# Performance work log

Measured on AMD Instinct MI355X. Metric: run time of the kernel, lower is better.

Reference implementation:

```python
import jax, jax.numpy as jnp
import numpy as np

N = 50000
NEG_SLOPE = 0.2
EPS = 1e-16


def add_self_loops(edge_index, n):
    loop = jnp.arange(n, dtype=edge_index.dtype)
    src = jnp.concatenate([edge_index[0], loop])
    dst = jnp.concatenate([edge_index[1], loop])
    return src, dst


def gat_conv(x, src, dst, W, att_src, att_dst, bias, n):
    # x: [N, F_in]; W: [F_in, H*D]; att_*: [H, D]; bias: [H*D]
    H, D = att_src.shape
    h = (x @ W).reshape(n, H, D)                      # [N, H, D]
    a_src = jnp.einsum('nhd,hd->nh', h, att_src)      # [N, H]
    a_dst = jnp.einsum('nhd,hd->nh', h, att_dst)
    e = jax.nn.leaky_relu(a_src[src] + a_dst[dst], NEG_SLOPE)  # [E, H]
    # softmax over incoming edges per destination node, per head
    m = jax.ops.segment_max(e, dst, num_segments=n)   # [N, H]
    ex = jnp.exp(e - m[dst])
    s = jax.ops.segment_sum(ex, dst, num_segments=n)
    alpha = ex / (s[dst] + EPS)                       # [E, H]
    msg = h[src] * alpha[:, :, None]                  # [E, H, D]
    out = jax.ops.segment_sum(msg, dst, num_segments=n)
    return out.reshape(n, H * D) + bias


def gcn_conv(x, src, dst, W, bias, n):
    h = x @ W                                         # [N, C]
    deg = jax.ops.segment_sum(jnp.ones_like(src, dtype=h.dtype), dst, num_segments=n)
    dinv = jnp.where(deg > 0, jax.lax.rsqrt(deg), 0.0)
    norm = dinv[src] * dinv[dst]                      # [E]
    out = jax.ops.segment_sum(h[src] * norm[:, None], dst, num_segments=n)
    return out + bias


def setup_inputs() -> dict:
    key = jax.random.key(0)
    ks = jax.random.split(key, 12)
    F_in, hid, heads, ncls = 128, 32, 8, 8
    d2 = hid // 2  # 16
    E = 500000
    x = jax.random.normal(ks[0], (N, F_in), dtype=jnp.float32)
    edge_index = jax.random.randint(ks[1], (2, E), 0, N, dtype=jnp.int32)
    sc = lambda k, sh: jax.random.normal(k, sh, dtype=jnp.float32) * 0.05
    return {
        'x': x, 'edge_index': edge_index,
        'W1': sc(ks[2], (F_in, heads * hid)),
        'att_src1': sc(ks[3], (heads, hid)), 'att_dst1': sc(ks[4], (heads, hid)),
        'b1': jnp.zeros((heads * hid,), jnp.float32),
        'W2': sc(ks[5], (heads * hid, heads * d2)),
        'att_src2': sc(ks[6], (heads, d2)), 'att_dst2': sc(ks[7], (heads, d2)),
        'b2': jnp.zeros((heads * d2,), jnp.float32),
        'Wg': sc(ks[8], (heads * d2, ncls)),
        'bg': jnp.zeros((ncls,), jnp.float32),
    }


def reference(x, edge_index, W1, att_src1, att_dst1, b1, W2, att_src2, att_dst2, b2, Wg, bg):
    src, dst = add_self_loops(edge_index, N)
    h = gat_conv(x, src, dst, W1, att_src1, att_dst1, b1, N)
    h = jax.nn.relu(h)
    h = gat_conv(h, src, dst, W2, att_src2, att_dst2, b2, N)
    h = jax.nn.relu(h)
    return gcn_conv(h, src, dst, Wg, bg, N)
```

## Files before the change

kernel.cpp:

```cpp
#include <hip/hip_runtime.h>
#include <hip/hip_bf16.h>


typedef __attribute__((ext_vector_type(8))) short bf16x8;
typedef __attribute__((ext_vector_type(4))) float f32x4;


__global__ __launch_bounds__(256) void zero_deg_kernel(int* __restrict__ deg, int n) {
    int i = blockIdx.x * 256 + threadIdx.x;
    if (i < n) deg[i] = 0;
}

__global__ __launch_bounds__(256) void hist_kernel(const int* __restrict__ ei, int E, int Etot,
                                                   int* __restrict__ deg) {
    int e = blockIdx.x * 256 + threadIdx.x;
    if (e >= Etot) return;
    int d = (e < E) ? ei[E + e] : (e - E);
    atomicAdd(&deg[d], 1);
}

__global__ __launch_bounds__(256) void scanA_kernel(const int* __restrict__ deg,
                                                    int* __restrict__ off,
                                                    int* __restrict__ bsum, int n) {
    __shared__ int buf[256];
    int t = threadIdx.x;
    int i = blockIdx.x * 256 + t;
    int v = (i < n) ? deg[i] : 0;
    buf[t] = v;
    __syncthreads();
    #pragma unroll
    for (int st = 1; st < 256; st <<= 1) {
        int x = (t >= st) ? buf[t - st] : 0;
        __syncthreads();
        buf[t] += x;
        __syncthreads();
    }
    if (i < n) off[i + 1] = buf[t];
    if (t == 255) bsum[blockIdx.x] = buf[255];
}

__global__ __launch_bounds__(256) void scanB_kernel(int* __restrict__ bsum, int nb) {
    __shared__ int buf[256];
    int t = threadIdx.x;
    int v = (t < nb) ? bsum[t] : 0;
    buf[t] = v;
    __syncthreads();
    #pragma unroll
    for (int st = 1; st < 256; st <<= 1) {
        int x = (t >= st) ? buf[t - st] : 0;
        __syncthreads();
        buf[t] += x;
        __syncthreads();
    }
    if (t < nb) bsum[t] = buf[t] - v;
}

__global__ __launch_bounds__(256) void scanC_kernel(const int* __restrict__ deg,
                                                    int* __restrict__ off,
                                                    const int* __restrict__ bsum,
                                                    int* __restrict__ cur,
                                                    float* __restrict__ dinv, int n) {
    int i = blockIdx.x * 256 + threadIdx.x;
    if (i < n) {
        int o = off[i + 1] + bsum[blockIdx.x];
        off[i + 1] = o;
        cur[i] = o - deg[i];
        dinv[i] = rsqrtf((float)deg[i]);
    }
    if (i == 0) off[0] = 0;
}

__global__ __launch_bounds__(256) void scatter_kernel(const int* __restrict__ ei, int E, int Etot,
                                                      int* __restrict__ cur,
                                                      int* __restrict__ ssrc) {
    int e = blockIdx.x * 256 + threadIdx.x;
    if (e >= Etot) return;
    int s, d;
    if (e < E) { s = ei[e]; d = ei[E + e]; }
    else       { s = e - E; d = e - E; }
    int pos = atomicAdd(&cur[d], 1);
    ssrc[pos] = s;
}


__global__ __launch_bounds__(256) void cvt_bf16_kernel(const float* __restrict__ in,
                                                       ushort* __restrict__ outb, int count) {
    int i = (blockIdx.x * 256 + threadIdx.x) * 4;
    if (i >= count) return;
    float4 v = *reinterpret_cast<const float4*>(in + i);
    ushort4 u;
    __hip_bfloat16 b0 = __float2bfloat16(v.x); u.x = *reinterpret_cast<ushort*>(&b0);
    __hip_bfloat16 b1 = __float2bfloat16(v.y); u.y = *reinterpret_cast<ushort*>(&b1);
    __hip_bfloat16 b2 = __float2bfloat16(v.z); u.z = *reinterpret_cast<ushort*>(&b2);
    __hip_bfloat16 b3 = __float2bfloat16(v.w); u.w = *reinterpret_cast<ushort*>(&b3);
    *reinterpret_cast<ushort4*>(outb + i) = u;
}

template <int K, int NC>
__global__ __launch_bounds__(256) void wtrans_kernel(const float* __restrict__ W,
                                                     ushort* __restrict__ Wt) {
    int t = blockIdx.x * 256 + threadIdx.x;
    if (t >= K * NC) return;
    int nn = t / K, k = t % K;
    __hip_bfloat16 b = __float2bfloat16(W[(size_t)k * NC + nn]);
    Wt[t] = *reinterpret_cast<ushort*>(&b);
}


template <int K, int D>
__global__ __launch_bounds__(256) void wprep_kernel(const float* __restrict__ W,
                                                    const float* __restrict__ att_s,
                                                    const float* __restrict__ att_d,
                                                    float* __restrict__ ws,
                                                    float* __restrict__ wd) {
    int t = blockIdx.x * 256 + threadIdx.x;
    if (t >= K * 8) return;
    int k = t >> 3, h = t & 7;
    const float* wrow = W + (size_t)k * (8 * D) + h * D;
    const float* as = att_s + h * D;
    const float* ad = att_d + h * D;
    float s1 = 0.f, s2 = 0.f;
    #pragma unroll
    for (int d = 0; d < D; d += 4) {
        float4 wv = *reinterpret_cast<const float4*>(wrow + d);
        float4 av = *reinterpret_cast<const float4*>(as + d);
        float4 dv = *reinterpret_cast<const float4*>(ad + d);
        s1 += wv.x * av.x + wv.y * av.y + wv.z * av.z + wv.w * av.w;
        s2 += wv.x * dv.x + wv.y * dv.y + wv.z * dv.z + wv.w * dv.w;
    }
    ws[t] = s1;
    wd[t] = s2;
}

template <int K>
__global__ __launch_bounds__(256) void adots_kernel(const float* __restrict__ X,
                                                    const float* __restrict__ ws,
                                                    const float* __restrict__ wd,
                                                    float* __restrict__ a_s,
                                                    float* __restrict__ a_d, int n) {
    int gid = blockIdx.x * 256 + threadIdx.x;
    if (gid >= n * 8) return;
    int node = gid >> 3, h = gid & 7;
    const float* xp = X + (size_t)node * K;
    float s1 = 0.f, s2 = 0.f;
    #pragma unroll 4
    for (int k = 0; k < K; k += 4) {
        float4 xv = *reinterpret_cast<const float4*>(xp + k);
        s1 += xv.x * ws[(k + 0) * 8 + h] + xv.y * ws[(k + 1) * 8 + h] +
              xv.z * ws[(k + 2) * 8 + h] + xv.w * ws[(k + 3) * 8 + h];
        s2 += xv.x * wd[(k + 0) * 8 + h] + xv.y * wd[(k + 1) * 8 + h] +
              xv.z * wd[(k + 2) * 8 + h] + xv.w * wd[(k + 3) * 8 + h];
    }
    a_s[gid] = s1;
    a_d[gid] = s2;
}


template <int K, int NC, int BN>
__global__ __launch_bounds__(256) void mfma_gemm_kernel(const ushort* __restrict__ Ab,
                                                        const ushort* __restrict__ Bt,
                                                        ushort* __restrict__ Cb, int M) {
    constexpr int BM = 128, BK = 32;
    constexpr int FN = BN / 32;
    __shared__ ushort As[BM * BK];
    __shared__ ushort Bs[BN * BK];
    const int tid = threadIdx.x;
    const int lane = tid & 63;
    const int wid = tid >> 6;
    const int bm = blockIdx.y * BM;
    const int bn = blockIdx.x * BN;
    const int wm = (wid >> 1) * 64;
    const int wn = (wid & 1) * (BN / 2);
    const int l15 = lane & 15;
    const int l4 = lane >> 4;
    f32x4 zero4 = {0.f, 0.f, 0.f, 0.f};
    f32x4 acc[4][FN];
    #pragma unroll
    for (int i = 0; i < 4; ++i)
        #pragma unroll
        for (int j = 0; j < FN; ++j) acc[i][j] = zero4;

    for (int k0 = 0; k0 < K; k0 += BK) {
        #pragma unroll
        for (int p = 0; p < 2; ++p) {
            int ci = tid + p * 256;
            int r = ci >> 2, c = ci & 3;
            int row = bm + r;
            uint4 v = make_uint4(0, 0, 0, 0);
            if (row < M) v = *reinterpret_cast<const uint4*>(&Ab[(size_t)row * K + k0 + c * 8]);
            *reinterpret_cast<uint4*>(&As[r * BK + c * 8]) = v;
        }
        #pragma unroll
        for (int p = 0; p < BN / 64; ++p) {
            int ci = tid + p * 256;
            int r = ci >> 2, c = ci & 3;
            uint4 v = *reinterpret_cast<const uint4*>(&Bt[(size_t)(bn + r) * K + k0 + c * 8]);
            *reinterpret_cast<uint4*>(&Bs[r * BK + c * 8]) = v;
        }
        __syncthreads();
        bf16x8 af[4], bfr[FN];
        #pragma unroll
        for (int i = 0; i < 4; ++i)
            af[i] = *reinterpret_cast<const bf16x8*>(&As[(wm + 16 * i + l15) * BK + l4 * 8]);
        #pragma unroll
        for (int j = 0; j < FN; ++j)
            bfr[j] = *reinterpret_cast<const bf16x8*>(&Bs[(wn + 16 * j + l15) * BK + l4 * 8]);
        #pragma unroll
        for (int i = 0; i < 4; ++i)
            #pragma unroll
            for (int j = 0; j < FN; ++j)
                acc[i][j] = __builtin_amdgcn_mfma_f32_16x16x32_bf16(af[i], bfr[j], acc[i][j], 0, 0, 0);
        __syncthreads();
    }
    #pragma unroll
    for (int i = 0; i < 4; ++i) {
        #pragma unroll
        for (int p = 0; p < 4; ++p) {
            int row = bm + wm + 16 * i + l4 * 4 + p;
            if (row < M) {
                #pragma unroll
                for (int j = 0; j < FN; ++j) {
                    __hip_bfloat16 hb = __float2bfloat16(acc[i][j][p]);
                    Cb[(size_t)row * NC + bn + wn + 16 * j + l15] = *reinterpret_cast<ushort*>(&hb);
                }
            }
        }
    }
}


#define LRELU_EXP(e) __expf((e) > 0.f ? (e) : 0.2f * (e))

__device__ __forceinline__ float4 bf4_to_f4(uint2 v) {
    float4 r;
    r.x = __uint_as_float((v.x & 0xFFFFu) << 16);
    r.y = __uint_as_float(v.x & 0xFFFF0000u);
    r.z = __uint_as_float((v.y & 0xFFFFu) << 16);
    r.w = __uint_as_float(v.y & 0xFFFF0000u);
    return r;
}

template <int C, int DH, bool DUAL>
__global__ __launch_bounds__(256) void gat_agg_kernel(const ushort* __restrict__ hfeat,
                                                      const float* __restrict__ a_src,
                                                      const float* __restrict__ a_dst,
                                                      const int* __restrict__ off,
                                                      const int* __restrict__ ssrc,
                                                      const float* __restrict__ bias,
                                                      float* __restrict__ outp,
                                                      ushort* __restrict__ outb, int n) {
    constexpr int LPN = C / 4;
    const int node = blockIdx.x * (256 / LPN) + threadIdx.x / LPN;
    if (node >= n) return;
    const int local = threadIdx.x & (LPN - 1);
    const int c0 = local * 4;
    const int h = c0 / DH;
    const float adst = a_dst[node * 8 + h];
    const int o0 = off[node], o1 = off[node + 1];
    float ax = 0.f, ay = 0.f, az = 0.f, aw = 0.f, ssum = 0.f;
    int i = o0;
    for (; i + 4 <= o1; i += 4) {
        int s0 = ssrc[i], s1 = ssrc[i + 1], s2 = ssrc[i + 2], s3 = ssrc[i + 3];
        float e0 = a_src[s0 * 8 + h], e1 = a_src[s1 * 8 + h];
        float e2 = a_src[s2 * 8 + h], e3 = a_src[s3 * 8 + h];
        uint2 r0 = *reinterpret_cast<const uint2*>(&hfeat[(size_t)s0 * C + c0]);
        uint2 r1 = *reinterpret_cast<const uint2*>(&hfeat[(size_t)s1 * C + c0]);
        uint2 r2 = *reinterpret_cast<const uint2*>(&hfeat[(size_t)s2 * C + c0]);
        uint2 r3 = *reinterpret_cast<const uint2*>(&hfeat[(size_t)s3 * C + c0]);
        float4 h0 = bf4_to_f4(r0), h1 = bf4_to_f4(r1), h2 = bf4_to_f4(r2), h3 = bf4_to_f4(r3);
        float v0 = LRELU_EXP(e0 + adst), v1 = LRELU_EXP(e1 + adst);
        float v2 = LRELU_EXP(e2 + adst), v3 = LRELU_EXP(e3 + adst);
        ssum += (v0 + v1) + (v2 + v3);
        ax += v0 * h0.x + v1 * h1.x + v2 * h2.x + v3 * h3.x;
        ay += v0 * h0.y + v1 * h1.y + v2 * h2.y + v3 * h3.y;
        az += v0 * h0.z + v1 * h1.z + v2 * h2.z + v3 * h3.z;
        aw += v0 * h0.w + v1 * h1.w + v2 * h2.w + v3 * h3.w;
    }
    for (; i < o1; ++i) {
        int s = ssrc[i];
        float e = a_src[s * 8 + h] + adst;
        float v = LRELU_EXP(e);
        uint2 rv = *reinterpret_cast<const uint2*>(&hfeat[(size_t)s * C + c0]);
        float4 hv = bf4_to_f4(rv);
        ssum += v;
        ax += v * hv.x; ay += v * hv.y; az += v * hv.z; aw += v * hv.w;
    }
    float sinv = 1.f / (ssum + 1e-16f);
    float4 bb = *reinterpret_cast<const float4*>(bias + c0);
    float4 o;
    o.x = fmaxf(ax * sinv + bb.x, 0.f);
    o.y = fmaxf(ay * sinv + bb.y, 0.f);
    o.z = fmaxf(az * sinv + bb.z, 0.f);
    o.w = fmaxf(aw * sinv + bb.w, 0.f);
    *reinterpret_cast<float4*>(&outp[(size_t)node * C + c0]) = o;
    if constexpr (DUAL) {
        ushort4 u;
        __hip_bfloat16 b0 = __float2bfloat16(o.x); u.x = *reinterpret_cast<ushort*>(&b0);
        __hip_bfloat16 b1 = __float2bfloat16(o.y); u.y = *reinterpret_cast<ushort*>(&b1);
        __hip_bfloat16 b2 = __float2bfloat16(o.z); u.z = *reinterpret_cast<ushort*>(&b2);
        __hip_bfloat16 b3 = __float2bfloat16(o.w); u.w = *reinterpret_cast<ushort*>(&b3);
        *reinterpret_cast<ushort4*>(&outb[(size_t)node * C + c0]) = u;
    }
}


__global__ __launch_bounds__(256) void gcn_gemm_kernel(const float* __restrict__ A,
                                                       const float* __restrict__ Wg,
                                                       float* __restrict__ g, int n) {
    __shared__ float W[128 * 8];
    for (int i = threadIdx.x; i < 1024; i += 256) W[i] = Wg[i];
    __syncthreads();
    int gid = blockIdx.x * 256 + threadIdx.x;
    if (gid >= n * 8) return;
    int node = gid >> 3, c = gid & 7;
    const float* ap = A + (size_t)node * 128;
    float acc = 0.f;
    #pragma unroll
    for (int k = 0; k < 128; k += 4) {
        float4 av = *reinterpret_cast<const float4*>(ap + k);
        acc += av.x * W[(k + 0) * 8 + c] + av.y * W[(k + 1) * 8 + c] +
               av.z * W[(k + 2) * 8 + c] + av.w * W[(k + 3) * 8 + c];
    }
    g[gid] = acc;
}

__global__ __launch_bounds__(256) void gcn_agg_kernel(const float* __restrict__ g,
                                                      const float* __restrict__ dinv,
                                                      const int* __restrict__ off,
                                                      const int* __restrict__ ssrc,
                                                      const float* __restrict__ bg,
                                                      float* __restrict__ outp, int n) {
    int gid = blockIdx.x * 256 + threadIdx.x;
    if (gid >= n * 8) return;
    int node = gid >> 3, c = gid & 7;
    int o0 = off[node], o1 = off[node + 1];
    float acc = 0.f;
    for (int i = o0; i < o1; ++i) {
        int s = ssrc[i];
        acc += g[(size_t)s * 8 + c] * dinv[s];
    }
    outp[gid] = acc * dinv[node] + bg[c];
}


extern "C" void kernel_launch(void* const* d_in, const int* in_sizes, int n_in,
                              void* d_out, int out_size, void* d_ws, size_t ws_size,
                              hipStream_t stream) {
    const float* x      = (const float*)d_in[0];
    const int*   ei     = (const int*)d_in[1];
    const float* W1     = (const float*)d_in[2];
    const float* att_s1 = (const float*)d_in[3];
    const float* att_d1 = (const float*)d_in[4];
    const float* b1     = (const float*)d_in[5];
    const float* W2     = (const float*)d_in[6];
    const float* att_s2 = (const float*)d_in[7];
    const float* att_d2 = (const float*)d_in[8];
    const float* b2     = (const float*)d_in[9];
    const float* Wg     = (const float*)d_in[10];
    const float* bg     = (const float*)d_in[11];
    float* out = (float*)d_out;

    const int n    = in_sizes[0] / 128;
    const int E    = in_sizes[1] / 2;
    const int Etot = E + n;

    float*  ws     = (float*)d_ws;
    float*  out1   = ws;
    float*  reg2   = out1 + (size_t)n * 256;
    float*  reg3   = reg2 + (size_t)n * 128;
    float*  reg4   = reg3 + (size_t)n * 128;
    float*  a_s    = reg4 + (size_t)n * 64;
    float*  a_d    = a_s + (size_t)n * 8;
    float*  g      = a_d + (size_t)n * 8;
    float*  dinv   = g + (size_t)n * 8;
    float*  w1s    = dinv + n;
    float*  w1d    = w1s + 1024;
    float*  w2s    = w1d + 1024;
    float*  w2d    = w2s + 2048;
    float*  w1t_f  = w2d + 2048;
    float*  w2t_f  = w1t_f + 16384;
    int*    off    = (int*)(w2t_f + 16384);
    int*    deg    = off + (n + 1);
    int*    cur    = deg + n;
    int*    ssrc   = cur + n;
    int*    bsum   = ssrc + Etot;

    ushort* out1b = (ushort*)reg2;
    ushort* h1b   = (ushort*)reg3;
    float*  out2  = reg3;
    ushort* xb    = (ushort*)reg4;
    ushort* h2b   = (ushort*)reg4;
    ushort* W1t   = (ushort*)w1t_f;
    ushort* W2t   = (ushort*)w2t_f;

    const dim3 b256(256);
    const int nch = (n + 255) / 256;

    zero_deg_kernel<<<nch, b256, 0, stream>>>(deg, n);
    hist_kernel<<<(Etot + 255) / 256, b256, 0, stream>>>(ei, E, Etot, deg);
    scanA_kernel<<<nch, b256, 0, stream>>>(deg, off, bsum, n);
    scanB_kernel<<<1, b256, 0, stream>>>(bsum, nch);
    scanC_kernel<<<nch, b256, 0, stream>>>(deg, off, bsum, cur, dinv, n);
    scatter_kernel<<<(Etot + 255) / 256, b256, 0, stream>>>(ei, E, Etot, cur, ssrc);

    wprep_kernel<128, 32><<<4, b256, 0, stream>>>(W1, att_s1, att_d1, w1s, w1d);
    wprep_kernel<256, 16><<<8, b256, 0, stream>>>(W2, att_s2, att_d2, w2s, w2d);
    cvt_bf16_kernel<<<(n * 128 / 4 + 255) / 256, b256, 0, stream>>>(x, xb, n * 128);
    wtrans_kernel<128, 256><<<(32768 + 255) / 256, b256, 0, stream>>>(W1, W1t);
    wtrans_kernel<256, 128><<<(32768 + 255) / 256, b256, 0, stream>>>(W2, W2t);

    adots_kernel<128><<<(n * 8 + 255) / 256, b256, 0, stream>>>(x, w1s, w1d, a_s, a_d, n);
    mfma_gemm_kernel<128, 256, 128><<<dim3(2, (n + 127) / 128), b256, 0, stream>>>(xb, W1t, h1b, n);
    gat_agg_kernel<256, 32, true><<<(n + 3) / 4, b256, 0, stream>>>(h1b, a_s, a_d, off, ssrc, b1, out1, out1b, n);

    adots_kernel<256><<<(n * 8 + 255) / 256, b256, 0, stream>>>(out1, w2s, w2d, a_s, a_d, n);
    mfma_gemm_kernel<256, 128, 64><<<dim3(2, (n + 127) / 128), b256, 0, stream>>>(out1b, W2t, h2b, n);
    gat_agg_kernel<128, 16, false><<<(n + 7) / 8, b256, 0, stream>>>(h2b, a_s, a_d, off, ssrc, b2, out2, nullptr, n);

    gcn_gemm_kernel<<<(n * 8 + 255) / 256, b256, 0, stream>>>(out2, Wg, g, n);
    gcn_agg_kernel<<<(n * 8 + 255) / 256, b256, 0, stream>>>(g, dinv, off, ssrc, bg, out, n);
}
```

Baseline: 280.8 us.

## Use bf16 intermediates everywhere and cooperatively load edge indices in GAT aggregation

The GAT aggregation kernels now write only bf16 outputs. The attention-dot and GCN GEMM kernels read bf16 activations instead of the fp32 copies, which removes the fp32 out1/out2 buffers and halves their read and write traffic. The edge loop in aggregation changes too: the lanes of each head group load a chunk of source indices and attention scores together and broadcast them with shuffles, so each lane no longer loads every index and score redundantly. The cost is extra bf16 rounding in the attention logits and the GCN input, plus shuffle overhead.

```diff
diff --git a/kernel.cpp b/kernel.cpp
--- a/kernel.cpp
+++ b/kernel.cpp
@@ -82,6 +82,15 @@
     ssrc[pos] = s;
 }
 
+
+__device__ __forceinline__ float4 bf4_to_f4(uint2 v) {
+    float4 r;
+    r.x = __uint_as_float((v.x & 0xFFFFu) << 16);
+    r.y = __uint_as_float(v.x & 0xFFFF0000u);
+    r.z = __uint_as_float((v.y & 0xFFFFu) << 16);
+    r.w = __uint_as_float(v.y & 0xFFFF0000u);
+    return r;
+}
 
 __global__ __launch_bounds__(256) void cvt_bf16_kernel(const float* __restrict__ in,
                                                        ushort* __restrict__ outb, int count) {
@@ -133,7 +142,7 @@
 }
 
 template <int K>
-__global__ __launch_bounds__(256) void adots_kernel(const float* __restrict__ X,
+__global__ __launch_bounds__(256) void adots_kernel(const ushort* __restrict__ Xb,
                                                     const float* __restrict__ ws,
                                                     const float* __restrict__ wd,
                                                     float* __restrict__ a_s,
@@ -141,15 +150,21 @@
     int gid = blockIdx.x * 256 + threadIdx.x;
     if (gid >= n * 8) return;
     int node = gid >> 3, h = gid & 7;
-    const float* xp = X + (size_t)node * K;
+    const ushort* xp = Xb + (size_t)node * K;
     float s1 = 0.f, s2 = 0.f;
     #pragma unroll 4
-    for (int k = 0; k < K; k += 4) {
-        float4 xv = *reinterpret_cast<const float4*>(xp + k);
-        s1 += xv.x * ws[(k + 0) * 8 + h] + xv.y * ws[(k + 1) * 8 + h] +
-              xv.z * ws[(k + 2) * 8 + h] + xv.w * ws[(k + 3) * 8 + h];
-        s2 += xv.x * wd[(k + 0) * 8 + h] + xv.y * wd[(k + 1) * 8 + h] +
-              xv.z * wd[(k + 2) * 8 + h] + xv.w * wd[(k + 3) * 8 + h];
+    for (int k = 0; k < K; k += 8) {
+        uint4 v = *reinterpret_cast<const uint4*>(xp + k);
+        float4 x0 = bf4_to_f4(make_uint2(v.x, v.y));
+        float4 x1 = bf4_to_f4(make_uint2(v.z, v.w));
+        s1 += x0.x * ws[(k + 0) * 8 + h] + x0.y * ws[(k + 1) * 8 + h] +
+              x0.z * ws[(k + 2) * 8 + h] + x0.w * ws[(k + 3) * 8 + h] +
+              x1.x * ws[(k + 4) * 8 + h] + x1.y * ws[(k + 5) * 8 + h] +
+              x1.z * ws[(k + 6) * 8 + h] + x1.w * ws[(k + 7) * 8 + h];
+        s2 += x0.x * wd[(k + 0) * 8 + h] + x0.y * wd[(k + 1) * 8 + h] +
+              x0.z * wd[(k + 2) * 8 + h] + x0.w * wd[(k + 3) * 8 + h] +
+              x1.x * wd[(k + 4) * 8 + h] + x1.y * wd[(k + 5) * 8 + h] +
+              x1.z * wd[(k + 6) * 8 + h] + x1.w * wd[(k + 7) * 8 + h];
     }
     a_s[gid] = s1;
     a_d[gid] = s2;
@@ -231,80 +246,71 @@
 
 #define LRELU_EXP(e) __expf((e) > 0.f ? (e) : 0.2f * (e))
 
-__device__ __forceinline__ float4 bf4_to_f4(uint2 v) {
-    float4 r;
-    r.x = __uint_as_float((v.x & 0xFFFFu) << 16);
-    r.y = __uint_as_float(v.x & 0xFFFF0000u);
-    r.z = __uint_as_float((v.y & 0xFFFFu) << 16);
-    r.w = __uint_as_float(v.y & 0xFFFF0000u);
-    return r;
-}
-
-template <int C, int DH, bool DUAL>
+template <int C, int DH>
 __global__ __launch_bounds__(256) void gat_agg_kernel(const ushort* __restrict__ hfeat,
                                                       const float* __restrict__ a_src,
                                                       const float* __restrict__ a_dst,
                                                       const int* __restrict__ off,
                                                       const int* __restrict__ ssrc,
                                                       const float* __restrict__ bias,
-                                                      float* __restrict__ outp,
                                                       ushort* __restrict__ outb, int n) {
     constexpr int LPN = C / 4;
+    constexpr int GS = DH / 4;
     const int node = blockIdx.x * (256 / LPN) + threadIdx.x / LPN;
     if (node >= n) return;
     const int local = threadIdx.x & (LPN - 1);
     const int c0 = local * 4;
     const int h = c0 / DH;
+    const int subl = local & (GS - 1);
     const float adst = a_dst[node * 8 + h];
     const int o0 = off[node], o1 = off[node + 1];
     float ax = 0.f, ay = 0.f, az = 0.f, aw = 0.f, ssum = 0.f;
     int i = o0;
-    for (; i + 4 <= o1; i += 4) {
-        int s0 = ssrc[i], s1 = ssrc[i + 1], s2 = ssrc[i + 2], s3 = ssrc[i + 3];
-        float e0 = a_src[s0 * 8 + h], e1 = a_src[s1 * 8 + h];
-        float e2 = a_src[s2 * 8 + h], e3 = a_src[s3 * 8 + h];
-        uint2 r0 = *reinterpret_cast<const uint2*>(&hfeat[(size_t)s0 * C + c0]);
-        uint2 r1 = *reinterpret_cast<const uint2*>(&hfeat[(size_t)s1 * C + c0]);
-        uint2 r2 = *reinterpret_cast<const uint2*>(&hfeat[(size_t)s2 * C + c0]);
-        uint2 r3 = *reinterpret_cast<const uint2*>(&hfeat[(size_t)s3 * C + c0]);
-        float4 h0 = bf4_to_f4(r0), h1 = bf4_to_f4(r1), h2 = bf4_to_f4(r2), h3 = bf4_to_f4(r3);
-        float v0 = LRELU_EXP(e0 + adst), v1 = LRELU_EXP(e1 + adst);
-        float v2 = LRELU_EXP(e2 + adst), v3 = LRELU_EXP(e3 + adst);
-        ssum += (v0 + v1) + (v2 + v3);
-        ax += v0 * h0.x + v1 * h1.x + v2 * h2.x + v3 * h3.x;
-        ay += v0 * h0.y + v1 * h1.y + v2 * h2.y + v3 * h3.y;
-        az += v0 * h0.z + v1 * h1.z + v2 * h2.z + v3 * h3.z;
-        aw += v0 * h0.w + v1 * h1.w + v2 * h2.w + v3 * h3.w;
+    const int nfull = o0 + ((o1 - o0) / GS) * GS;
+    for (; i < nfull; i += GS) {
+        int smy = ssrc[i + subl];
+        float e = a_src[smy * 8 + h] + adst;
+        float evmy = LRELU_EXP(e);
+        int sj[GS];
+        #pragma unroll
+        for (int j = 0; j < GS; ++j) sj[j] = __shfl(smy, j, GS);
+        uint2 rv[GS];
+        #pragma unroll
+        for (int j = 0; j < GS; ++j)
+            rv[j] = *reinterpret_cast<const uint2*>(&hfeat[(size_t)sj[j] * C + c0]);
+        #pragma unroll
+        for (int j = 0; j < GS; ++j) {
+            float ev = __shfl(evmy, j, GS);
+            float4 hv = bf4_to_f4(rv[j]);
+            ssum += ev;
+            ax += ev * hv.x; ay += ev * hv.y; az += ev * hv.z; aw += ev * hv.w;
+        }
     }
     for (; i < o1; ++i) {
         int s = ssrc[i];
         float e = a_src[s * 8 + h] + adst;
         float v = LRELU_EXP(e);
-        uint2 rv = *reinterpret_cast<const uint2*>(&hfeat[(size_t)s * C + c0]);
-        float4 hv = bf4_to_f4(rv);
+        uint2 rvv = *reinterpret_cast<const uint2*>(&hfeat[(size_t)s * C + c0]);
+        float4 hv = bf4_to_f4(rvv);
         ssum += v;
         ax += v * hv.x; ay += v * hv.y; az += v * hv.z; aw += v * hv.w;
     }
     float sinv = 1.f / (ssum + 1e-16f);
     float4 bb = *reinterpret_cast<const float4*>(bias + c0);
-    float4 o;
-    o.x = fmaxf(ax * sinv + bb.x, 0.f);
-    o.y = fmaxf(ay * sinv + bb.y, 0.f);
-    o.z = fmaxf(az * sinv + bb.z, 0.f);
-    o.w = fmaxf(aw * sinv + bb.w, 0.f);
-    *reinterpret_cast<float4*>(&outp[(size_t)node * C + c0]) = o;
-    if constexpr (DUAL) {
-        ushort4 u;
-        __hip_bfloat16 b0 = __float2bfloat16(o.x); u.x = *reinterpret_cast<ushort*>(&b0);
-        __hip_bfloat16 b1 = __float2bfloat16(o.y); u.y = *reinterpret_cast<ushort*>(&b1);
-        __hip_bfloat16 b2 = __float2bfloat16(o.z); u.z = *reinterpret_cast<ushort*>(&b2);
-        __hip_bfloat16 b3 = __float2bfloat16(o.w); u.w = *reinterpret_cast<ushort*>(&b3);
-        *reinterpret_cast<ushort4*>(&outb[(size_t)node * C + c0]) = u;
-    }
-}
-
-
-__global__ __launch_bounds__(256) void gcn_gemm_kernel(const float* __restrict__ A,
+    float ox = fmaxf(ax * sinv + bb.x, 0.f);
+    float oy = fmaxf(ay * sinv + bb.y, 0.f);
+    float oz = fmaxf(az * sinv + bb.z, 0.f);
+    float ow = fmaxf(aw * sinv + bb.w, 0.f);
+    ushort4 u;
+    __hip_bfloat16 b0 = __float2bfloat16(ox); u.x = *reinterpret_cast<ushort*>(&b0);
+    __hip_bfloat16 b1 = __float2bfloat16(oy); u.y = *reinterpret_cast<ushort*>(&b1);
+    __hip_bfloat16 b2 = __float2bfloat16(oz); u.z = *reinterpret_cast<ushort*>(&b2);
+    __hip_bfloat16 b3 = __float2bfloat16(ow); u.w = *reinterpret_cast<ushort*>(&b3);
+    *reinterpret_cast<ushort4*>(&outb[(size_t)node * C + c0]) = u;
+}
+
+
+__global__ __launch_bounds__(256) void gcn_gemm_kernel(const ushort* __restrict__ Ab,
                                                        const float* __restrict__ Wg,
                                                        float* __restrict__ g, int n) {
     __shared__ float W[128 * 8];
@@ -313,13 +319,17 @@
     int gid = blockIdx.x * 256 + threadIdx.x;
     if (gid >= n * 8) return;
     int node = gid >> 3, c = gid & 7;
-    const float* ap = A + (size_t)node * 128;
+    const ushort* ap = Ab + (size_t)node * 128;
     float acc = 0.f;
     #pragma unroll
-    for (int k = 0; k < 128; k += 4) {
-        float4 av = *reinterpret_cast<const float4*>(ap + k);
-        acc += av.x * W[(k + 0) * 8 + c] + av.y * W[(k + 1) * 8 + c] +
-               av.z * W[(k + 2) * 8 + c] + av.w * W[(k + 3) * 8 + c];
+    for (int k = 0; k < 128; k += 8) {
+        uint4 v = *reinterpret_cast<const uint4*>(ap + k);
+        float4 x0 = bf4_to_f4(make_uint2(v.x, v.y));
+        float4 x1 = bf4_to_f4(make_uint2(v.z, v.w));
+        acc += x0.x * W[(k + 0) * 8 + c] + x0.y * W[(k + 1) * 8 + c] +
+               x0.z * W[(k + 2) * 8 + c] + x0.w * W[(k + 3) * 8 + c] +
+               x1.x * W[(k + 4) * 8 + c] + x1.y * W[(k + 5) * 8 + c] +
+               x1.z * W[(k + 6) * 8 + c] + x1.w * W[(k + 7) * 8 + c];
     }
     g[gid] = acc;
 }
@@ -364,32 +374,31 @@
     const int E    = in_sizes[1] / 2;
     const int Etot = E + n;
 
-    float*  ws     = (float*)d_ws;
-    float*  out1   = ws;
-    float*  reg2   = out1 + (size_t)n * 256;
-    float*  reg3   = reg2 + (size_t)n * 128;
-    float*  reg4   = reg3 + (size_t)n * 128;
-    float*  a_s    = reg4 + (size_t)n * 64;
-    float*  a_d    = a_s + (size_t)n * 8;
-    float*  g      = a_d + (size_t)n * 8;
-    float*  dinv   = g + (size_t)n * 8;
-    float*  w1s    = dinv + n;
-    float*  w1d    = w1s + 1024;
-    float*  w2s    = w1d + 1024;
-    float*  w2d    = w2s + 2048;
-    float*  w1t_f  = w2d + 2048;
-    float*  w2t_f  = w1t_f + 16384;
-    int*    off    = (int*)(w2t_f + 16384);
-    int*    deg    = off + (n + 1);
-    int*    cur    = deg + n;
-    int*    ssrc   = cur + n;
-    int*    bsum   = ssrc + Etot;
-
-    ushort* out1b = (ushort*)reg2;
-    ushort* h1b   = (ushort*)reg3;
-    float*  out2  = reg3;
-    ushort* xb    = (ushort*)reg4;
-    ushort* h2b   = (ushort*)reg4;
+    float*  wsp   = (float*)d_ws;
+    float*  regA  = wsp;
+    float*  regB  = regA + (size_t)n * 128;
+    float*  regC  = regB + (size_t)n * 128;
+    float*  a_s   = regC + (size_t)n * 64;
+    float*  a_d   = a_s + (size_t)n * 8;
+    float*  g     = a_d + (size_t)n * 8;
+    float*  dinv  = g + (size_t)n * 8;
+    float*  w1s   = dinv + n;
+    float*  w1d   = w1s + 1024;
+    float*  w2s   = w1d + 1024;
+    float*  w2d   = w2s + 2048;
+    float*  w1t_f = w2d + 2048;
+    float*  w2t_f = w1t_f + 16384;
+    int*    off   = (int*)(w2t_f + 16384);
+    int*    deg   = off + (n + 1);
+    int*    cur   = deg + n;
+    int*    ssrc  = cur + n;
+    int*    bsum  = ssrc + Etot;
+
+    ushort* h1b   = (ushort*)regA;
+    ushort* out2b = (ushort*)regA;
+    ushort* out1b = (ushort*)regB;
+    ushort* xb    = (ushort*)regC;
+    ushort* h2b   = (ushort*)regC;
     ushort* W1t   = (ushort*)w1t_f;
     ushort* W2t   = (ushort*)w2t_f;
 
@@ -409,14 +418,14 @@
     wtrans_kernel<128, 256><<<(32768 + 255) / 256, b256, 0, stream>>>(W1, W1t);
     wtrans_kernel<256, 128><<<(32768 + 255) / 256, b256, 0, stream>>>(W2, W2t);
 
-    adots_kernel<128><<<(n * 8 + 255) / 256, b256, 0, stream>>>(x, w1s, w1d, a_s, a_d, n);
+    adots_kernel<128><<<(n * 8 + 255) / 256, b256, 0, stream>>>(xb, w1s, w1d, a_s, a_d, n);
     mfma_gemm_kernel<128, 256, 128><<<dim3(2, (n + 127) / 128), b256, 0, stream>>>(xb, W1t, h1b, n);
-    gat_agg_kernel<256, 32, true><<<(n + 3) / 4, b256, 0, stream>>>(h1b, a_s, a_d, off, ssrc, b1, out1, out1b, n);
-
-    adots_kernel<256><<<(n * 8 + 255) / 256, b256, 0, stream>>>(out1, w2s, w2d, a_s, a_d, n);
+    gat_agg_kernel<256, 32><<<(n + 3) / 4, b256, 0, stream>>>(h1b, a_s, a_d, off, ssrc, b1, out1b, n);
+
+    adots_kernel<256><<<(n * 8 + 255) / 256, b256, 0, stream>>>(out1b, w2s, w2d, a_s, a_d, n);
     mfma_gemm_kernel<256, 128, 64><<<dim3(2, (n + 127) / 128), b256, 0, stream>>>(out1b, W2t, h2b, n);
-    gat_agg_kernel<128, 16, false><<<(n + 7) / 8, b256, 0, stream>>>(h2b, a_s, a_d, off, ssrc, b2, out2, nullptr, n);
-
-    gcn_gemm_kernel<<<(n * 8 + 255) / 256, b256, 0, stream>>>(out2, Wg, g, n);
+    gat_agg_kernel<128, 16><<<(n + 7) / 8, b256, 0, stream>>>(h2b, a_s, a_d, off, ssrc, b2, out2b, n);
+
+    gcn_gemm_kernel<<<(n * 8 + 255) / 256, b256, 0, stream>>>(out2b, Wg, g, n);
     gcn_agg_kernel<<<(n * 8 + 255) / 256, b256, 0, stream>>>(g, dinv, off, ssrc, bg, out, n);
 }
```

Measured after the change: 263.3 us. 1.07x faster.
